# Performance work log

Measured on AMD Instinct MI355X. Metric: run time of the kernel, lower is better.

The kernel has to match this reference:

```python
import jax, jax.numpy as jnp
import numpy as np

SELF_DIM = 6   # self_state_dim
HID = 50       # lstm_hidden_dim


def setup_inputs() -> dict:
    key = jax.random.key(0)
    ks = jax.random.split(key, 16)
    B, N, D = 8192, 64, 13  # batch, num humans, joint-state length

    def w(k, shape):
        # kaiming-ish init, stored as [in, out] so forward is x @ W + b
        return jax.random.normal(k, shape, jnp.float32) / jnp.sqrt(jnp.float32(shape[0]))

    z = lambda n: jnp.zeros((n,), jnp.float32)
    return {
        "state": jax.random.normal(ks[0], (B, N, D), jnp.float32),
        # mlp1: 13 -> 150 -> 100, last_relu=True
        "mlp1_w1": w(ks[1], (13, 150)),  "mlp1_b1": z(150),
        "mlp1_w2": w(ks[2], (150, 100)), "mlp1_b2": z(100),
        # attention: 200 -> 100 -> 100 -> 1 (no relu on last)
        "attn_w1": w(ks[3], (200, 100)), "attn_b1": z(100),
        "attn_w2": w(ks[4], (100, 100)), "attn_b2": z(100),
        "attn_w3": w(ks[5], (100, 1)),   "attn_b3": z(1),
        # LSTM(input=7, hidden=50), torch gate order i,f,g,o
        "lstm_wih": w(ks[6], (7, 4 * HID)),
        "lstm_whh": w(ks[7], (HID, 4 * HID)),
        "lstm_bih": z(4 * HID), "lstm_bhh": z(4 * HID),
        # mlp: 56 -> 150 -> 100 -> 100 -> 1
        "mlp_w1": w(ks[8], (SELF_DIM + HID, 150)), "mlp_b1": z(150),
        "mlp_w2": w(ks[9], (150, 100)),            "mlp_b2": z(100),
        "mlp_w3": w(ks[10], (100, 100)),           "mlp_b3": z(100),
        "mlp_w4": w(ks[11], (100, 1)),             "mlp_b4": z(1),
    }


def reference(state, mlp1_w1, mlp1_b1, mlp1_w2, mlp1_b2,
              attn_w1, attn_b1, attn_w2, attn_b2, attn_w3, attn_b3,
              lstm_wih, lstm_whh, lstm_bih, lstm_bhh,
              mlp_w1, mlp_b1, mlp_w2, mlp_b2, mlp_w3, mlp_b3, mlp_w4, mlp_b4):
    relu = jax.nn.relu
    B, N, D = state.shape
    self_state = state[:, 0, :SELF_DIM]      # [B, 6]
    human_state = state[:, :, SELF_DIM:]     # [B, N, 7]

    # mlp1 over all B*N per-human joint-state rows (last_relu=True)
    flat = state.reshape(B * N, D)
    m1 = relu(relu(flat @ mlp1_w1 + mlp1_b1) @ mlp1_w2 + mlp1_b2)   # [B*N, 100]

    # mean-pooled global state, broadcast back per human, concat, attention score
    gdim = m1.shape[-1]
    global_state = jnp.mean(m1.reshape(B, N, gdim), axis=1, keepdims=True)
    global_state = jnp.broadcast_to(global_state, (B, N, gdim)).reshape(B * N, gdim)
    a_in = jnp.concatenate([m1, global_state], axis=1)               # [B*N, 200]
    scores = (relu(relu(a_in @ attn_w1 + attn_b1) @ attn_w2 + attn_b2) @ attn_w3 + attn_b3)
    scores = scores.reshape(B, N)
    # NOTE: in the original torch code `scores` only feed `rerank_human_state`,
    # which is never consumed (dead code) -- the LSTM runs on the UNSORTED
    # human_state. We keep the score computation for fidelity; the per-sample
    # argsort/gather is dropped since it does not affect the output.

    # LSTM over the N humans (batch_first in torch, h0=c0=0)
    xs = jnp.transpose(human_state, (1, 0, 2))   # [N, B, 7]
    h0 = jnp.zeros((B, HID), state.dtype)

    def step(carry, x_t):
        h, c = carry
        gates = x_t @ lstm_wih + h @ lstm_whh + lstm_bih + lstm_bhh  # [B, 4H]
        i, f, g, o = jnp.split(gates, 4, axis=-1)
        c = jax.nn.sigmoid(f) * c + jax.nn.sigmoid(i) * jnp.tanh(g)
        h = jax.nn.sigmoid(o) * jnp.tanh(c)
        return (h, c), None

    (hn, _cn), _ = jax.lax.scan(step, (h0, h0), xs)

    # value head on [self_state, h_n]
    joint = jnp.concatenate([self_state, hn], axis=1)   # [B, 56]
    x = relu(joint @ mlp_w1 + mlp_b1)
    x = relu(x @ mlp_w2 + mlp_b2)
    x = relu(x @ mlp_w3 + mlp_b3)
    value = x @ mlp_w4 + mlp_b4                          # [B, 1]
    return value
```

## Files before the change

### kernel.cpp

```cpp
#include <hip/hip_runtime.h>

typedef __attribute__((ext_vector_type(8))) short short8;
typedef __attribute__((ext_vector_type(4))) float f32x4;
union frag_u { short8 v; unsigned short u[8]; };

__device__ __forceinline__ float bf2f(unsigned short b) {
  unsigned int u = ((unsigned int)b) << 16;
  float f; __builtin_memcpy(&f, &u, 4); return f;
}
__device__ __forceinline__ unsigned short f2bf(float f) {
  unsigned int u; __builtin_memcpy(&u, &f, 4);
  return (unsigned short)((u + 0x7FFFu + ((u >> 16) & 1u)) >> 16);
}
__device__ __forceinline__ unsigned short hi_of(float f) { return f2bf(f); }
__device__ __forceinline__ unsigned short lo_of(float f) {
  unsigned short h = f2bf(f); return f2bf(f - bf2f(h));
}
__device__ __forceinline__ float sigm(float x) {
  return __builtin_amdgcn_rcpf(1.f + __expf(-x));
}
__device__ __forceinline__ float tanh_(float x) {
  return 1.f - 2.f * __builtin_amdgcn_rcpf(1.f + __expf(2.f * x));
}

__device__ __forceinline__ float dpp_xor1(float x) {
  union { float f; int i; } a, r; a.f = x;
  r.i = __builtin_amdgcn_update_dpp(0, a.i, 0xB1, 0xF, 0xF, true);
  return r.f;
}
__device__ __forceinline__ float dpp_xor2(float x) {
  union { float f; int i; } a, r; a.f = x;
  r.i = __builtin_amdgcn_update_dpp(0, a.i, 0x4E, 0xF, 0xF, true);
  return r.f;
}

__global__ void detect_dtype_kernel(const unsigned short* s, int* flag) {
  int i = threadIdx.x;
  unsigned short v = s[2 * i];
  int e = (v >> 7) & 0xFF;
  unsigned long long m = __ballot(e < 100 || e > 140);
  if (i == 0) *flag = (__popcll(m) >= 16) ? 1 : 0;
}

template <int AS, typename GetB, typename GetW>
__device__ __forceinline__ void mfma_layer(const unsigned short* sA, float* sG,
    int wave, int col, int quad, int kc_n, int ntiles, int N, GetB getb, GetW getw)
{
  for (int tile = wave; tile < ntiles; tile += 16) {
    int n = tile * 16 + col;
    float b = (n < N) ? getb(n) : 0.f;
    f32x4 acc = {b, b, b, b};
    for (int kc = 0; kc < kc_n; ++kc) {
      short8 a = *(const short8*)&sA[col * AS + kc * 32 + quad * 8];
      frag_u w;
      #pragma unroll
      for (int j = 0; j < 8; ++j) {
        int k = kc * 32 + quad * 8 + j;
        w.u[j] = (n < N) ? getw(k, n) : (unsigned short)0;
      }
      acc = __builtin_amdgcn_mfma_f32_16x16x32_bf16(a, w.v, acc, 0, 0, 0);
    }
    *(f32x4*)&sG[n * 20 + quad * 4] = acc;
  }
}

template <int AS, bool LO>
__device__ __forceinline__ void relu_fill(const float* sG, unsigned short* sA,
                                          int tid, int N, int loOff, int Kpad) {
  for (int idx = tid; idx < 16 * Kpad; idx += 1024) {
    int m = idx & 15, n = idx >> 4;
    unsigned short v = 0;
    if (n < N) {
      v = f2bf(fmaxf(sG[n * 20 + m], 0.f));
    } else if (LO && n >= loOff && n < loOff + N) {
      float x = fmaxf(sG[(n - loOff) * 20 + m], 0.f);
      v = lo_of(x);
    }
    sA[m * AS + n] = v;
  }
}

template <bool F32>
__global__ __launch_bounds__(1024, 8) void value_net_kernel(
    const void* state_, const void* wih_, const void* whh_,
    const void* bih_, const void* bhh_,
    const void* w1_, const void* b1_, const void* w2_, const void* b2_,
    const void* w3_, const void* b3_, const void* w4_, const void* b4_,
    void* out_, const int* flag)
{
  if (flag && *flag != (F32 ? 1 : 0)) return;

  constexpr int AS = F32 ? 328 : 168;
  constexpr int KC = F32 ? 6 : 4;

  __shared__ __align__(16) unsigned short sA[2][16 * AS];
  __shared__ __align__(16) float sG[208 * 20];

  const unsigned short* st16 = (const unsigned short*)state_;
  const float*          stf  = (const float*)state_;

  const int tid  = threadIdx.x;
  const int wave = tid >> 6;
  const int lane = tid & 63;
  const int col  = lane & 15;
  const int quad = lane >> 4;
  const int r0   = blockIdx.x * 16;

  {
    unsigned int* a32 = (unsigned int*)&sA[0][0];
    constexpr int ZT = 16 * AS;
    #pragma unroll
    for (int i = 0; i < (ZT + 1023) / 1024; ++i) {
      int idx = tid + i * 1024;
      if (idx < ZT) a32[idx] = 0;
    }
  }

  auto W_lstm = [&](int k, int n) -> unsigned short {
    if constexpr (!F32) {
      const unsigned short* wih = (const unsigned short*)wih_;
      const unsigned short* whh = (const unsigned short*)whh_;
      if (k < 7)   return wih[k * 200 + n];
      if (k < 57)  return whh[(k - 7) * 200 + n];
      if (k < 107) return whh[(k - 57) * 200 + n];
      return (unsigned short)0;
    } else {
      const float* wih = (const float*)wih_;
      const float* whh = (const float*)whh_;
      if (k < 7)   return hi_of(wih[k * 200 + n]);
      if (k < 14)  return hi_of(wih[(k - 7) * 200 + n]);
      if (k < 21)  return lo_of(wih[(k - 14) * 200 + n]);
      if (k < 71)  return hi_of(whh[(k - 21) * 200 + n]);
      if (k < 121) return hi_of(whh[(k - 71) * 200 + n]);
      if (k < 171) return lo_of(whh[(k - 121) * 200 + n]);
      return (unsigned short)0;
    }
  };
  auto ldf = [&](const void* p, int i) -> float {
    if constexpr (F32) return ((const float*)p)[i];
    else               return bf2f(((const unsigned short*)p)[i]);
  };

  const bool hasTile = (wave < 13);
  frag_u wf[KC];
  float  wb = 0.f;
  if (hasTile) {
    int nn = wave * 16 + col;
    int no = (nn < 200) ? ((nn & 3) * 50 + (nn >> 2)) : 0;
    #pragma unroll
    for (int kc = 0; kc < KC; ++kc) {
      #pragma unroll
      for (int j = 0; j < 8; ++j) {
        int k = kc * 32 + quad * 8 + j;
        wf[kc].u[j] = (nn < 200) ? W_lstm(k, no) : (unsigned short)0;
      }
    }
    wb = (nn < 200) ? (ldf(bih_, no) + ldf(bhh_, no)) : 0.f;
  }

  const int  u_   = wave * 4 + (col >> 2);
  const int  mm   = quad * 4 + (col & 3);
  const bool iact = hasTile && (u_ < 50);
  float c_ = 0.f, hf = 0.f;

  const bool isx = (tid >= 832) && (tid < 944);
  const int  xm = (tid - 832) / 7, xd = (tid - 832) - ((tid - 832) / 7) * 7;
  auto xgidx = [&](int t) -> size_t { return (size_t)(r0 + xm) * 832 + t * 13 + 6 + xd; };
  auto xwrite = [&](unsigned short* sAw, float fv, unsigned short bv) {
    if constexpr (!F32) { sAw[xm * AS + xd] = bv; }
    else {
      unsigned short h = f2bf(fv);
      sAw[xm * AS + xd] = h; sAw[xm * AS + 14 + xd] = h;
      sAw[xm * AS + 7 + xd] = f2bf(fv - bf2f(h));
    }
  };
  unsigned short xv16 = 0; float xvf = 0.f;

  __syncthreads();
  if (isx) {
    if constexpr (!F32) { xwrite(&sA[0][0], 0.f, st16[xgidx(0)]); xv16 = st16[xgidx(1)]; }
    else                { xwrite(&sA[0][0], stf[xgidx(0)], 0);    xvf  = stf[xgidx(1)]; }
  }
  __syncthreads();

  for (int t = 0; t < 64; ++t) {
    const unsigned short* sAr = &sA[t & 1][0];
    unsigned short*       sAw = &sA[(t & 1) ^ 1][0];

    if (hasTile) {
      short8 a[KC];
      #pragma unroll
      for (int kc = 0; kc < KC; ++kc)
        a[kc] = *(const short8*)&sAr[col * AS + kc * 32 + quad * 8];
      f32x4 acc = {wb, wb, wb, wb};
      #pragma unroll
      for (int kc = 0; kc < KC; ++kc)
        acc = __builtin_amdgcn_mfma_f32_16x16x32_bf16(a[kc], wf[kc].v, acc, 0, 0, 0);

      f32x4 s1, m1, s2, w;
      #pragma unroll
      for (int r = 0; r < 4; ++r) s1[r] = dpp_xor1(acc[r]);
      const bool b0 = (lane & 1);
      m1[0] = b0 ? s1[1] : acc[0];
      m1[1] = b0 ? acc[1] : s1[0];
      m1[2] = b0 ? s1[3] : acc[2];
      m1[3] = b0 ? acc[3] : s1[2];
      #pragma unroll
      for (int r = 0; r < 4; ++r) s2[r] = dpp_xor2(m1[r]);
      const bool b1 = (lane & 2);
      w[0] = b1 ? s2[2] : m1[0];
      w[1] = b1 ? s2[3] : m1[1];
      w[2] = b1 ? m1[2] : s2[0];
      w[3] = b1 ? m1[3] : s2[1];

      if (iact) {
        float cc = sigm(w[1]) * c_ + sigm(w[0]) * tanh_(w[2]);
        c_ = cc;
        float h = sigm(w[3]) * tanh_(cc);
        if (t < 63) {
          unsigned short hb = f2bf(h);
          unsigned short hl = f2bf(h - bf2f(hb));
          if constexpr (!F32) {
            sAw[mm * AS + 7 + u_] = hb; sAw[mm * AS + 57 + u_] = hl;
          } else {
            sAw[mm * AS + 21 + u_] = hb; sAw[mm * AS + 121 + u_] = hb;
            sAw[mm * AS + 71 + u_] = hl;
          }
        } else hf = h;
      }
    } else if (isx && t < 63) {
      if constexpr (!F32) xwrite(sAw, 0.f, xv16); else xwrite(sAw, xvf, 0);
      if (t < 62) { if constexpr (!F32) xv16 = st16[xgidx(t + 2)]; else xvf = stf[xgidx(t + 2)]; }
    }
    __syncthreads();
  }

  unsigned short* sA0 = &sA[0][0];
  {
    unsigned int* a32 = (unsigned int*)sA0;
    #pragma unroll
    for (int i = 0; i < (16 * AS / 2 + 1023) / 1024; ++i) {
      int idx = tid + i * 1024;
      if (idx < 16 * AS / 2) a32[idx] = 0;
    }
  }
  __syncthreads();
  if (iact) {
    unsigned short hb = f2bf(hf);
    unsigned short hl = f2bf(hf - bf2f(hb));
    sA0[mm * AS + 6 + u_] = hb;
    if constexpr (!F32) sA0[mm * AS + 56 + u_] = hl; else sA0[mm * AS + 62 + u_] = hl;
  }
  if (tid < 96) {
    int m = tid / 6, d = tid - (tid / 6) * 6;
    if constexpr (!F32) sA0[m * AS + d] = st16[(size_t)(r0 + m) * 832 + d];
    else {
      float f = stf[(size_t)(r0 + m) * 832 + d];
      sA0[m * AS + d] = hi_of(f); sA0[m * AS + 56 + d] = lo_of(f);
    }
  }
  __syncthreads();

  mfma_layer<AS>(sA0, sG, wave, col, quad, 4, 10, 150,
    [&](int n) { return ldf(b1_, n); },
    [&](int k, int n) -> unsigned short {
      if constexpr (!F32) {
        const unsigned short* w1 = (const unsigned short*)w1_;
        if (k < 56)  return w1[k * 150 + n];
        if (k < 106) return w1[(k - 50) * 150 + n];
        return (unsigned short)0;
      } else {
        const float* w1 = (const float*)w1_;
        if (k < 56)  return hi_of(w1[k * 150 + n]);
        if (k < 112) return hi_of(w1[(k - 56) * 150 + n]);
        return (unsigned short)0;
      }
    });
  __syncthreads();
  if constexpr (!F32) relu_fill<AS, false>(sG, sA0, tid, 150, 160, 160);
  else                relu_fill<AS, true >(sG, sA0, tid, 150, 150, 320);
  __syncthreads();

  mfma_layer<AS>(sA0, sG, wave, col, quad, F32 ? 10 : 5, 7, 100,
    [&](int n) { return ldf(b2_, n); },
    [&](int k, int n) -> unsigned short {
      if constexpr (!F32) {
        const unsigned short* w2 = (const unsigned short*)w2_;
        return (k < 150) ? w2[k * 100 + n] : (unsigned short)0;
      } else {
        const float* w2 = (const float*)w2_;
        if (k < 150) return hi_of(w2[k * 100 + n]);
        if (k < 300) return hi_of(w2[(k - 150) * 100 + n]);
        return (unsigned short)0;
      }
    });
  __syncthreads();
  if constexpr (!F32) relu_fill<AS, false>(sG, sA0, tid, 100, 128, 128);
  else                relu_fill<AS, true >(sG, sA0, tid, 100, 100, 224);
  __syncthreads();

  mfma_layer<AS>(sA0, sG, wave, col, quad, F32 ? 7 : 4, 7, 100,
    [&](int n) { return ldf(b3_, n); },
    [&](int k, int n) -> unsigned short {
      if constexpr (!F32) {
        const unsigned short* w3 = (const unsigned short*)w3_;
        return (k < 100) ? w3[k * 100 + n] : (unsigned short)0;
      } else {
        const float* w3 = (const float*)w3_;
        if (k < 100) return hi_of(w3[k * 100 + n]);
        if (k < 200) return hi_of(w3[(k - 100) * 100 + n]);
        return (unsigned short)0;
      }
    });
  __syncthreads();

  if (tid < 256) {
    int m = tid >> 4, j0 = tid & 15;
    float s = 0.f;
    for (int j = j0; j < 100; j += 16)
      s += fmaxf(sG[j * 20 + m], 0.f) * ldf(w4_, j);
    s += __shfl_xor(s, 8); s += __shfl_xor(s, 4);
    s += __shfl_xor(s, 2); s += __shfl_xor(s, 1);
    if (j0 == 0) {
      float v = s + ldf(b4_, 0);
      if constexpr (!F32) ((unsigned short*)out_)[r0 + m] = f2bf(v);
      else                ((float*)out_)[r0 + m] = v;
    }
  }
}

extern "C" void kernel_launch(void* const* d_in, const int* in_sizes, int n_in,
                              void* d_out, int out_size, void* d_ws, size_t ws_size,
                              hipStream_t stream) {
  (void)n_in; (void)out_size;
  const void* state = d_in[0];
  const void* wih = d_in[11]; const void* whh = d_in[12];
  const void* bih = d_in[13]; const void* bhh = d_in[14];
  const void* w1  = d_in[15]; const void* b1  = d_in[16];
  const void* w2  = d_in[17]; const void* b2  = d_in[18];
  const void* w3  = d_in[19]; const void* b3  = d_in[20];
  const void* w4  = d_in[21]; const void* b4  = d_in[22];

  const long long F32B  = 8192LL * 64 * 13 * 4;
  const long long BF16B = 8192LL * 64 * 13 * 2;
  long long sz = in_sizes ? (long long)in_sizes[0] : -1;

  if (sz == F32B) {
    value_net_kernel<true><<<dim3(512), dim3(1024), 0, stream>>>(
        state, wih, whh, bih, bhh, w1, b1, w2, b2, w3, b3, w4, b4, d_out,
        (const int*)nullptr);
  } else if (sz == BF16B) {
    value_net_kernel<false><<<dim3(512), dim3(1024), 0, stream>>>(
        state, wih, whh, bih, bhh, w1, b1, w2, b2, w3, b3, w4, b4, d_out,
        (const int*)nullptr);
  } else if (ws_size >= sizeof(int)) {
    int* flag = (int*)d_ws;
    detect_dtype_kernel<<<dim3(1), dim3(64), 0, stream>>>(
        (const unsigned short*)state, flag);
    value_net_kernel<false><<<dim3(512), dim3(1024), 0, stream>>>(
        state, wih, whh, bih, bhh, w1, b1, w2, b2, w3, b3, w4, b4, d_out, flag);
    value_net_kernel<true><<<dim3(512), dim3(1024), 0, stream>>>(
        state, wih, whh, bih, bhh, w1, b1, w2, b2, w3, b3, w4, b4, d_out, flag);
  } else {
    value_net_kernel<false><<<dim3(512), dim3(1024), 0, stream>>>(
        state, wih, whh, bih, bhh, w1, b1, w2, b2, w3, b3, w4, b4, d_out,
        (const int*)nullptr);
  }
}
```

Before: 232.7 us.

## Split LSTM and value head into separate kernels with 256-thread LSTM blocks

Splits the fused kernel into an LSTM kernel and a value-head MLP kernel that talk through a global h_n buffer. The LSTM kernel now uses 4 waves per block, each owning 3-4 gate tiles with their weights held in registers. It also preloads all 64 timesteps of human input into shared memory, so the serial per-step loop no longer waits on global memory. The aim is to cut per-step barrier cost across 16 waves, keep the serial recurrence busy, and let more LSTM blocks share a CU, at the cost of a second launch, a global round trip for h_n, and more registers per thread.

Result: slower. 285.8 us (+22.8%).

```diff
diff --git a/kernel.cpp b/kernel.cpp
--- a/kernel.cpp
+++ b/kernel.cpp
@@ -33,6 +33,8 @@
   r.i = __builtin_amdgcn_update_dpp(0, a.i, 0x4E, 0xF, 0xF, true);
   return r.f;
 }
+
+__device__ float gH[8192 * 50];
 
 __global__ void detect_dtype_kernel(const unsigned short* s, int* flag) {
   int i = threadIdx.x;
@@ -42,51 +44,10 @@
   if (i == 0) *flag = (__popcll(m) >= 16) ? 1 : 0;
 }
 
-template <int AS, typename GetB, typename GetW>
-__device__ __forceinline__ void mfma_layer(const unsigned short* sA, float* sG,
-    int wave, int col, int quad, int kc_n, int ntiles, int N, GetB getb, GetW getw)
-{
-  for (int tile = wave; tile < ntiles; tile += 16) {
-    int n = tile * 16 + col;
-    float b = (n < N) ? getb(n) : 0.f;
-    f32x4 acc = {b, b, b, b};
-    for (int kc = 0; kc < kc_n; ++kc) {
-      short8 a = *(const short8*)&sA[col * AS + kc * 32 + quad * 8];
-      frag_u w;
-      #pragma unroll
-      for (int j = 0; j < 8; ++j) {
-        int k = kc * 32 + quad * 8 + j;
-        w.u[j] = (n < N) ? getw(k, n) : (unsigned short)0;
-      }
-      acc = __builtin_amdgcn_mfma_f32_16x16x32_bf16(a, w.v, acc, 0, 0, 0);
-    }
-    *(f32x4*)&sG[n * 20 + quad * 4] = acc;
-  }
-}
-
-template <int AS, bool LO>
-__device__ __forceinline__ void relu_fill(const float* sG, unsigned short* sA,
-                                          int tid, int N, int loOff, int Kpad) {
-  for (int idx = tid; idx < 16 * Kpad; idx += 1024) {
-    int m = idx & 15, n = idx >> 4;
-    unsigned short v = 0;
-    if (n < N) {
-      v = f2bf(fmaxf(sG[n * 20 + m], 0.f));
-    } else if (LO && n >= loOff && n < loOff + N) {
-      float x = fmaxf(sG[(n - loOff) * 20 + m], 0.f);
-      v = lo_of(x);
-    }
-    sA[m * AS + n] = v;
-  }
-}
-
 template <bool F32>
-__global__ __launch_bounds__(1024, 8) void value_net_kernel(
+__global__ __launch_bounds__(256) void lstm_kernel(
     const void* state_, const void* wih_, const void* whh_,
-    const void* bih_, const void* bhh_,
-    const void* w1_, const void* b1_, const void* w2_, const void* b2_,
-    const void* w3_, const void* b3_, const void* w4_, const void* b4_,
-    void* out_, const int* flag)
+    const void* bih_, const void* bhh_, const int* flag)
 {
   if (flag && *flag != (F32 ? 1 : 0)) return;
 
@@ -94,7 +55,7 @@
   constexpr int KC = F32 ? 6 : 4;
 
   __shared__ __align__(16) unsigned short sA[2][16 * AS];
-  __shared__ __align__(16) float sG[208 * 20];
+  __shared__ __align__(16) unsigned short sX[64 * 16 * 8 * (F32 ? 2 : 1)];
 
   const unsigned short* st16 = (const unsigned short*)state_;
   const float*          stf  = (const float*)state_;
@@ -110,9 +71,27 @@
     unsigned int* a32 = (unsigned int*)&sA[0][0];
     constexpr int ZT = 16 * AS;
     #pragma unroll
-    for (int i = 0; i < (ZT + 1023) / 1024; ++i) {
-      int idx = tid + i * 1024;
+    for (int i = 0; i < (ZT + 255) / 256; ++i) {
+      int idx = tid + i * 256;
       if (idx < ZT) a32[idx] = 0;
+    }
+  }
+
+  for (int idx = tid; idx < 1024; idx += 256) {
+    int t = idx & 63, r = idx >> 6;
+    size_t g = (size_t)(r0 + r) * 832 + (size_t)t * 13 + 6;
+    int base = (t * 16 + r) * 8;
+    if constexpr (!F32) {
+      #pragma unroll
+      for (int d = 0; d < 7; ++d) sX[base + d] = st16[g + d];
+    } else {
+      #pragma unroll
+      for (int d = 0; d < 7; ++d) {
+        float f = stf[g + d];
+        unsigned short h = f2bf(f);
+        sX[2 * (base + d) + 0] = h;
+        sX[2 * (base + d) + 1] = f2bf(f - bf2f(h));
+      }
     }
   }
 
@@ -141,103 +120,179 @@
     else               return bf2f(((const unsigned short*)p)[i]);
   };
 
-  const bool hasTile = (wave < 13);
-  frag_u wf[KC];
-  float  wb = 0.f;
-  if (hasTile) {
-    int nn = wave * 16 + col;
+  const int nmine = (wave == 0) ? 4 : 3;
+  frag_u wf[4][KC];
+  float  wb[4];
+  #pragma unroll
+  for (int i = 0; i < 4; ++i) {
+    if (i >= nmine) continue;
+    int nn = (wave + 4 * i) * 16 + col;
     int no = (nn < 200) ? ((nn & 3) * 50 + (nn >> 2)) : 0;
     #pragma unroll
     for (int kc = 0; kc < KC; ++kc) {
       #pragma unroll
       for (int j = 0; j < 8; ++j) {
         int k = kc * 32 + quad * 8 + j;
-        wf[kc].u[j] = (nn < 200) ? W_lstm(k, no) : (unsigned short)0;
-      }
-    }
-    wb = (nn < 200) ? (ldf(bih_, no) + ldf(bhh_, no)) : 0.f;
-  }
-
-  const int  u_   = wave * 4 + (col >> 2);
-  const int  mm   = quad * 4 + (col & 3);
-  const bool iact = hasTile && (u_ < 50);
-  float c_ = 0.f, hf = 0.f;
-
-  const bool isx = (tid >= 832) && (tid < 944);
-  const int  xm = (tid - 832) / 7, xd = (tid - 832) - ((tid - 832) / 7) * 7;
-  auto xgidx = [&](int t) -> size_t { return (size_t)(r0 + xm) * 832 + t * 13 + 6 + xd; };
-  auto xwrite = [&](unsigned short* sAw, float fv, unsigned short bv) {
-    if constexpr (!F32) { sAw[xm * AS + xd] = bv; }
-    else {
-      unsigned short h = f2bf(fv);
+        wf[i][kc].u[j] = (nn < 200) ? W_lstm(k, no) : (unsigned short)0;
+      }
+    }
+    wb[i] = (nn < 200) ? (ldf(bih_, no) + ldf(bhh_, no)) : 0.f;
+  }
+
+  const int mm = quad * 4 + (col & 3);
+  float c_[4] = {0.f, 0.f, 0.f, 0.f}, hreg[4] = {0.f, 0.f, 0.f, 0.f};
+
+  const bool isx = tid < 112;
+  const int  xm = tid / 7, xd = tid - (tid / 7) * 7;
+  auto xfeed = [&](unsigned short* sAw, int t) {
+    int base = (t * 16 + xm) * 8 + xd;
+    if constexpr (!F32) {
+      sAw[xm * AS + xd] = sX[base];
+    } else {
+      unsigned short h = sX[2 * base + 0], l = sX[2 * base + 1];
       sAw[xm * AS + xd] = h; sAw[xm * AS + 14 + xd] = h;
-      sAw[xm * AS + 7 + xd] = f2bf(fv - bf2f(h));
+      sAw[xm * AS + 7 + xd] = l;
     }
   };
-  unsigned short xv16 = 0; float xvf = 0.f;
-
-  __syncthreads();
-  if (isx) {
-    if constexpr (!F32) { xwrite(&sA[0][0], 0.f, st16[xgidx(0)]); xv16 = st16[xgidx(1)]; }
-    else                { xwrite(&sA[0][0], stf[xgidx(0)], 0);    xvf  = stf[xgidx(1)]; }
-  }
+
+  __syncthreads();
+  if (isx) xfeed(&sA[0][0], 0);
   __syncthreads();
 
   for (int t = 0; t < 64; ++t) {
     const unsigned short* sAr = &sA[t & 1][0];
     unsigned short*       sAw = &sA[(t & 1) ^ 1][0];
 
-    if (hasTile) {
-      short8 a[KC];
+    short8 a[KC];
+    #pragma unroll
+    for (int kc = 0; kc < KC; ++kc)
+      a[kc] = *(const short8*)&sAr[col * AS + kc * 32 + quad * 8];
+
+    #pragma unroll
+    for (int i = 0; i < 4; ++i) {
+      if (i < nmine) {
+        f32x4 acc = {wb[i], wb[i], wb[i], wb[i]};
+        #pragma unroll
+        for (int kc = 0; kc < KC; ++kc)
+          acc = __builtin_amdgcn_mfma_f32_16x16x32_bf16(a[kc], wf[i][kc].v, acc, 0, 0, 0);
+
+        f32x4 s1, m1, s2, w;
+        #pragma unroll
+        for (int r = 0; r < 4; ++r) s1[r] = dpp_xor1(acc[r]);
+        const bool b0 = (lane & 1);
+        m1[0] = b0 ? s1[1] : acc[0];
+        m1[1] = b0 ? acc[1] : s1[0];
+        m1[2] = b0 ? s1[3] : acc[2];
+        m1[3] = b0 ? acc[3] : s1[2];
+        #pragma unroll
+        for (int r = 0; r < 4; ++r) s2[r] = dpp_xor2(m1[r]);
+        const bool b1 = (lane & 2);
+        w[0] = b1 ? s2[2] : m1[0];
+        w[1] = b1 ? s2[3] : m1[1];
+        w[2] = b1 ? m1[2] : s2[0];
+        w[3] = b1 ? m1[3] : s2[1];
+
+        int u_ = (wave + 4 * i) * 4 + (col >> 2);
+        if (u_ < 50) {
+          float cc = sigm(w[1]) * c_[i] + sigm(w[0]) * tanh_(w[2]);
+          c_[i] = cc;
+          float h = sigm(w[3]) * tanh_(cc);
+          if (t < 63) {
+            unsigned short hb = f2bf(h);
+            unsigned short hl = f2bf(h - bf2f(hb));
+            if constexpr (!F32) {
+              sAw[mm * AS + 7 + u_] = hb; sAw[mm * AS + 57 + u_] = hl;
+            } else {
+              sAw[mm * AS + 21 + u_] = hb; sAw[mm * AS + 121 + u_] = hb;
+              sAw[mm * AS + 71 + u_] = hl;
+            }
+          } else hreg[i] = h;
+        }
+      }
+    }
+
+    if (isx && t < 63) xfeed(sAw, t + 1);
+    __syncthreads();
+  }
+
+  #pragma unroll
+  for (int i = 0; i < 4; ++i) {
+    if (i < nmine) {
+      int u_ = (wave + 4 * i) * 4 + (col >> 2);
+      if (u_ < 50) gH[(size_t)(r0 + mm) * 50 + u_] = hreg[i];
+    }
+  }
+}
+
+template <int AS, typename GetB, typename GetW>
+__device__ __forceinline__ void mfma_layer(const unsigned short* sA, float* sG,
+    int wave, int col, int quad, int kc_n, int ntiles, int N, GetB getb, GetW getw)
+{
+  for (int tile = wave; tile < ntiles; tile += 16) {
+    int n = tile * 16 + col;
+    float b = (n < N) ? getb(n) : 0.f;
+    f32x4 acc = {b, b, b, b};
+    for (int kc = 0; kc < kc_n; ++kc) {
+      short8 a = *(const short8*)&sA[col * AS + kc * 32 + quad * 8];
+      frag_u w;
       #pragma unroll
-      for (int kc = 0; kc < KC; ++kc)
-        a[kc] = *(const short8*)&sAr[col * AS + kc * 32 + quad * 8];
-      f32x4 acc = {wb, wb, wb, wb};
-      #pragma unroll
-      for (int kc = 0; kc < KC; ++kc)
-        acc = __builtin_amdgcn_mfma_f32_16x16x32_bf16(a[kc], wf[kc].v, acc, 0, 0, 0);
-
-      f32x4 s1, m1, s2, w;
-      #pragma unroll
-      for (int r = 0; r < 4; ++r) s1[r] = dpp_xor1(acc[r]);
-      const bool b0 = (lane & 1);
-      m1[0] = b0 ? s1[1] : acc[0];
-      m1[1] = b0 ? acc[1] : s1[0];
-      m1[2] = b0 ? s1[3] : acc[2];
-      m1[3] = b0 ? acc[3] : s1[2];
-      #pragma unroll
-      for (int r = 0; r < 4; ++r) s2[r] = dpp_xor2(m1[r]);
-      const bool b1 = (lane & 2);
-      w[0] = b1 ? s2[2] : m1[0];
-      w[1] = b1 ? s2[3] : m1[1];
-      w[2] = b1 ? m1[2] : s2[0];
-      w[3] = b1 ? m1[3] : s2[1];
-
-      if (iact) {
-        float cc = sigm(w[1]) * c_ + sigm(w[0]) * tanh_(w[2]);
-        c_ = cc;
-        float h = sigm(w[3]) * tanh_(cc);
-        if (t < 63) {
-          unsigned short hb = f2bf(h);
-          unsigned short hl = f2bf(h - bf2f(hb));
-          if constexpr (!F32) {
-            sAw[mm * AS + 7 + u_] = hb; sAw[mm * AS + 57 + u_] = hl;
-          } else {
-            sAw[mm * AS + 21 + u_] = hb; sAw[mm * AS + 121 + u_] = hb;
-            sAw[mm * AS + 71 + u_] = hl;
-          }
-        } else hf = h;
-      }
-    } else if (isx && t < 63) {
-      if constexpr (!F32) xwrite(sAw, 0.f, xv16); else xwrite(sAw, xvf, 0);
-      if (t < 62) { if constexpr (!F32) xv16 = st16[xgidx(t + 2)]; else xvf = stf[xgidx(t + 2)]; }
-    }
-    __syncthreads();
-  }
-
-  unsigned short* sA0 = &sA[0][0];
+      for (int j = 0; j < 8; ++j) {
+        int k = kc * 32 + quad * 8 + j;
+        w.u[j] = (n < N) ? getw(k, n) : (unsigned short)0;
+      }
+      acc = __builtin_amdgcn_mfma_f32_16x16x32_bf16(a, w.v, acc, 0, 0, 0);
+    }
+    *(f32x4*)&sG[n * 20 + quad * 4] = acc;
+  }
+}
+
+template <int AS, bool LO>
+__device__ __forceinline__ void relu_fill(const float* sG, unsigned short* sA,
+                                          int tid, int N, int loOff, int Kpad) {
+  for (int idx = tid; idx < 16 * Kpad; idx += 1024) {
+    int m = idx & 15, n = idx >> 4;
+    unsigned short v = 0;
+    if (n < N) {
+      v = f2bf(fmaxf(sG[n * 20 + m], 0.f));
+    } else if (LO && n >= loOff && n < loOff + N) {
+      float x = fmaxf(sG[(n - loOff) * 20 + m], 0.f);
+      v = lo_of(x);
+    }
+    sA[m * AS + n] = v;
+  }
+}
+
+template <bool F32>
+__global__ __launch_bounds__(1024, 8) void tail_kernel(
+    const void* state_,
+    const void* w1_, const void* b1_, const void* w2_, const void* b2_,
+    const void* w3_, const void* b3_, const void* w4_, const void* b4_,
+    void* out_, const int* flag)
+{
+  if (flag && *flag != (F32 ? 1 : 0)) return;
+
+  constexpr int AS = F32 ? 328 : 168;
+
+  __shared__ __align__(16) unsigned short sA[16 * AS];
+  __shared__ __align__(16) float sG[208 * 20];
+
+  const unsigned short* st16 = (const unsigned short*)state_;
+  const float*          stf  = (const float*)state_;
+
+  const int tid  = threadIdx.x;
+  const int wave = tid >> 6;
+  const int lane = tid & 63;
+  const int col  = lane & 15;
+  const int quad = lane >> 4;
+  const int r0   = blockIdx.x * 16;
+
+  auto ldf = [&](const void* p, int i) -> float {
+    if constexpr (F32) return ((const float*)p)[i];
+    else               return bf2f(((const unsigned short*)p)[i]);
+  };
+
   {
-    unsigned int* a32 = (unsigned int*)sA0;
+    unsigned int* a32 = (unsigned int*)sA;
     #pragma unroll
     for (int i = 0; i < (16 * AS / 2 + 1023) / 1024; ++i) {
       int idx = tid + i * 1024;
@@ -245,23 +300,26 @@
     }
   }
   __syncthreads();
-  if (iact) {
-    unsigned short hb = f2bf(hf);
-    unsigned short hl = f2bf(hf - bf2f(hb));
-    sA0[mm * AS + 6 + u_] = hb;
-    if constexpr (!F32) sA0[mm * AS + 56 + u_] = hl; else sA0[mm * AS + 62 + u_] = hl;
+
+  if (tid < 800) {
+    int m = tid & 15, u = tid >> 4;
+    float h = gH[(size_t)(r0 + m) * 50 + u];
+    unsigned short hb = f2bf(h);
+    unsigned short hl = f2bf(h - bf2f(hb));
+    sA[m * AS + 6 + u] = hb;
+    if constexpr (!F32) sA[m * AS + 56 + u] = hl; else sA[m * AS + 62 + u] = hl;
   }
   if (tid < 96) {
     int m = tid / 6, d = tid - (tid / 6) * 6;
-    if constexpr (!F32) sA0[m * AS + d] = st16[(size_t)(r0 + m) * 832 + d];
+    if constexpr (!F32) sA[m * AS + d] = st16[(size_t)(r0 + m) * 832 + d];
     else {
       float f = stf[(size_t)(r0 + m) * 832 + d];
-      sA0[m * AS + d] = hi_of(f); sA0[m * AS + 56 + d] = lo_of(f);
-    }
-  }
-  __syncthreads();
-
-  mfma_layer<AS>(sA0, sG, wave, col, quad, 4, 10, 150,
+      sA[m * AS + d] = hi_of(f); sA[m * AS + 56 + d] = lo_of(f);
+    }
+  }
+  __syncthreads();
+
+  mfma_layer<AS>(sA, sG, wave, col, quad, 4, 10, 150,
     [&](int n) { return ldf(b1_, n); },
     [&](int k, int n) -> unsigned short {
       if constexpr (!F32) {
@@ -277,11 +335,11 @@
       }
     });
   __syncthreads();
-  if constexpr (!F32) relu_fill<AS, false>(sG, sA0, tid, 150, 160, 160);
-  else                relu_fill<AS, true >(sG, sA0, tid, 150, 150, 320);
-  __syncthreads();
-
-  mfma_layer<AS>(sA0, sG, wave, col, quad, F32 ? 10 : 5, 7, 100,
+  if constexpr (!F32) relu_fill<AS, false>(sG, sA, tid, 150, 160, 160);
+  else                relu_fill<AS, true >(sG, sA, tid, 150, 150, 320);
+  __syncthreads();
+
+  mfma_layer<AS>(sA, sG, wave, col, quad, F32 ? 10 : 5, 7, 100,
     [&](int n) { return ldf(b2_, n); },
     [&](int k, int n) -> unsigned short {
       if constexpr (!F32) {
@@ -295,11 +353,11 @@
       }
     });
   __syncthreads();
-  if constexpr (!F32) relu_fill<AS, false>(sG, sA0, tid, 100, 128, 128);
-  else                relu_fill<AS, true >(sG, sA0, tid, 100, 100, 224);
-  __syncthreads();
-
-  mfma_layer<AS>(sA0, sG, wave, col, quad, F32 ? 7 : 4, 7, 100,
+  if constexpr (!F32) relu_fill<AS, false>(sG, sA, tid, 100, 128, 128);
+  else                relu_fill<AS, true >(sG, sA, tid, 100, 100, 224);
+  __syncthreads();
+
+  mfma_layer<AS>(sA, sG, wave, col, quad, F32 ? 7 : 4, 7, 100,
     [&](int n) { return ldf(b3_, n); },
     [&](int k, int n) -> unsigned short {
       if constexpr (!F32) {
@@ -346,24 +404,31 @@
   long long sz = in_sizes ? (long long)in_sizes[0] : -1;
 
   if (sz == F32B) {
-    value_net_kernel<true><<<dim3(512), dim3(1024), 0, stream>>>(
-        state, wih, whh, bih, bhh, w1, b1, w2, b2, w3, b3, w4, b4, d_out,
-        (const int*)nullptr);
+    lstm_kernel<true><<<dim3(512), dim3(256), 0, stream>>>(
+        state, wih, whh, bih, bhh, (const int*)nullptr);
+    tail_kernel<true><<<dim3(512), dim3(1024), 0, stream>>>(
+        state, w1, b1, w2, b2, w3, b3, w4, b4, d_out, (const int*)nullptr);
   } else if (sz == BF16B) {
-    value_net_kernel<false><<<dim3(512), dim3(1024), 0, stream>>>(
-        state, wih, whh, bih, bhh, w1, b1, w2, b2, w3, b3, w4, b4, d_out,
-        (const int*)nullptr);
+    lstm_kernel<false><<<dim3(512), dim3(256), 0, stream>>>(
+        state, wih, whh, bih, bhh, (const int*)nullptr);
+    tail_kernel<false><<<dim3(512), dim3(1024), 0, stream>>>(
+        state, w1, b1, w2, b2, w3, b3, w4, b4, d_out, (const int*)nullptr);
   } else if (ws_size >= sizeof(int)) {
     int* flag = (int*)d_ws;
     detect_dtype_kernel<<<dim3(1), dim3(64), 0, stream>>>(
         (const unsigned short*)state, flag);
-    value_net_kernel<false><<<dim3(512), dim3(1024), 0, stream>>>(
-        state, wih, whh, bih, bhh, w1, b1, w2, b2, w3, b3, w4, b4, d_out, flag);
-    value_net_kernel<true><<<dim3(512), dim3(1024), 0, stream>>>(
-        state, wih, whh, bih, bhh, w1, b1, w2, b2, w3, b3, w4, b4, d_out, flag);
+    lstm_kernel<false><<<dim3(512), dim3(256), 0, stream>>>(
+        state, wih, whh, bih, bhh, flag);
+    lstm_kernel<true><<<dim3(512), dim3(256), 0, stream>>>(
+        state, wih, whh, bih, bhh, flag);
+    tail_kernel<false><<<dim3(512), dim3(1024), 0, stream>>>(
+        state, w1, b1, w2, b2, w3, b3, w4, b4, d_out, flag);
+    tail_kernel<true><<<dim3(512), dim3(1024), 0, stream>>>(
+        state, w1, b1, w2, b2, w3, b3, w4, b4, d_out, flag);
   } else {
-    value_net_kernel<false><<<dim3(512), dim3(1024), 0, stream>>>(
-        state, wih, whh, bih, bhh, w1, b1, w2, b2, w3, b3, w4, b4, d_out,
-        (const int*)nullptr);
-  }
-}
+    lstm_kernel<false><<<dim3(512), dim3(256), 0, stream>>>(
+        state, wih, whh, bih, bhh, (const int*)nullptr);
+    tail_kernel<false><<<dim3(512), dim3(1024), 0, stream>>>(
+        state, w1, b1, w2, b2, w3, b3, w4, b4, d_out, (const int*)nullptr);
+  }
+}
```
